# Kernel tuning notes

Hardware: AMD Instinct MI355X
Metric: run time of the kernel (lower is better)

Reference implementation:

```python
import jax, jax.numpy as jnp
import numpy as np

N = 2_000_000
VOXEL_SIZE = (0.1, 0.1, 0.1)
PC_RANGE = (-50.0, -50.0, -5.0, 50.0, 50.0, 3.0)
NUM_BATCHES = 4


def setup_inputs() -> dict:
    key = jax.random.key(0)
    k1, k2 = jax.random.split(key)
    pmin = jnp.array(PC_RANGE[:3], dtype=jnp.float32)
    pmax = jnp.array(PC_RANGE[3:], dtype=jnp.float32)
    # points uniformly distributed over the configured point-cloud range
    points = jax.random.uniform(k1, (N, 3), dtype=jnp.float32, minval=pmin, maxval=pmax)
    batch_indices = jnp.sort(jax.random.randint(k2, (N,), 0, NUM_BATCHES, dtype=jnp.int32))
    return {"points": points, "batch_indices": batch_indices}


def reference(points, batch_indices):
    """Vectorized equivalent of PointVoxelizer.forward.

    Returns fixed-shape (jit-friendly) analogues of the torch outputs:
      voxel_coords   [N, 4] int32  [batch, z, y, x], padded rows = -1
      voxel_features [N, 3] float32 voxel centers, padded rows = 0
      point_to_voxel_map [N] int32, -1 for invalid points
      n_voxels       scalar int32, number of real (non-padding) voxels
    The per-batch torch.unique + offset concatenation is reproduced exactly by
    a single sorted unique over the combined hash batch*GRID + cell_hash,
    since unique sorts and the hash is lexicographic in (batch, x, y, z).
    """
    dtype = points.dtype
    vsize = jnp.array(VOXEL_SIZE, dtype=dtype)
    pmin = jnp.array(PC_RANGE[:3], dtype=dtype)
    pmax = jnp.array(PC_RANGE[3:], dtype=dtype)

    vc = jnp.floor((points - pmin) / vsize).astype(jnp.int32)  # [N,3] (x,y,z)
    grid = jnp.ceil((pmax - pmin) / vsize).astype(jnp.int32)   # [3] = (1000,1000,80)
    valid = jnp.all(vc >= 0, axis=1) & jnp.all(vc < grid, axis=1)  # [N]

    YZ = grid[1] * grid[2]
    GXYZ = grid[0] * YZ  # cells per batch element (8e7 < 2^31/NUM_BATCHES)
    cell_hash = vc[:, 0] * YZ + vc[:, 1] * grid[2] + vc[:, 2]
    SENTINEL = jnp.iinfo(jnp.int32).max
    combined = jnp.where(valid, batch_indices.astype(jnp.int32) * GXYZ + cell_hash, SENTINEL)

    uniq, inv = jnp.unique(combined, return_inverse=True, size=N, fill_value=SENTINEL)
    is_real = uniq != SENTINEL  # padding (and any invalid-point bucket) masked out

    point_to_voxel_map = jnp.where(valid, inv.reshape(-1).astype(jnp.int32), -1)

    b = uniq // GXYZ
    rem = uniq % GXYZ
    x = rem // YZ
    y = (rem % YZ) // grid[2]
    z = rem % grid[2]

    coords_bzyx = jnp.stack([b, z, y, x], axis=1).astype(jnp.int32)  # [N,4]
    voxel_coords = jnp.where(is_real[:, None], coords_bzyx, -1)

    xyz = jnp.stack([x, y, z], axis=1).astype(dtype)
    centers = pmin + (xyz + 0.5) * vsize
    voxel_features = jnp.where(is_real[:, None], centers, jnp.zeros((), dtype))

    n_voxels = is_real.sum().astype(jnp.int32)
    return voxel_coords, voxel_features, point_to_voxel_map, n_voxels
```

## Files before the change

### kernel.cpp

```cpp
#include <hip/hip_runtime.h>


namespace {

constexpr int GX = 1000, GY = 1000, GZ = 80;
constexpr int YZ = GY * GZ;
constexpr int GXYZ = GX * YZ;
constexpr int TOTAL_CELLS = GXYZ * 4;
constexpr int BBITS = 18;
constexpr int BCELLS = 1 << BBITS;
constexpr int NB = (TOTAL_CELLS + BCELLS - 1) >> BBITS;
constexpr int BWORDS = BCELLS / 32;
constexpr int NCHUNK = 512;
static_assert(NCHUNK % 64 == 0, "k2a wave scan");
static_assert(NB <= 2048, "1-block scans assume <=2048 elements");

constexpr size_t OFF_PK    = 8000000;
constexpr size_t OFF_POS   = 16000000;
constexpr size_t OFF_MVAL  = 24000000;
constexpr size_t OFF_DK    = 32000000;
constexpr size_t OFF_HIST  = 40000000;
constexpr size_t OFF_TOT   = 43000000;
constexpr size_t OFF_BOFF  = 43100000;
constexpr size_t OFF_DCNT  = 43200000;
constexpr size_t OFF_DRANK = 43300000;

__device__ __forceinline__ int sw(int w) {
  return ((w & 7) << 10) | (w >> 3);
}

__global__ void k1_keys_hist(const float* __restrict__ pts, const int* __restrict__ bi,
                             unsigned* __restrict__ upt, unsigned* __restrict__ hist,
                             int n, int cpb) {
  __shared__ unsigned h[NB];
  const int c = blockIdx.x;
  for (int b = threadIdx.x; b < NB; b += blockDim.x) h[b] = 0;
  __syncthreads();
  const int lo = c * cpb, hi = min(n, lo + cpb);
  for (int i = lo + threadIdx.x; i < hi; i += blockDim.x) {
    float px = pts[3 * i + 0], py = pts[3 * i + 1], pz = pts[3 * i + 2];
    int vx = (int)floorf((px + 50.0f) / 0.1f);
    int vy = (int)floorf((py + 50.0f) / 0.1f);
    int vz = (int)floorf((pz + 5.0f) / 0.1f);
    bool valid = (vx >= 0) & (vy >= 0) & (vz >= 0) & (vx < GX) & (vy < GY) & (vz < GZ);
    unsigned u = 0xFFFFFFFFu;
    if (valid) {
      u = (unsigned)(bi[i] * GXYZ + vx * YZ + vy * GZ + vz);
      atomicAdd(&h[u >> BBITS], 1u);
    }
    upt[i] = u;
  }
  __syncthreads();
  for (int b = threadIdx.x; b < NB; b += blockDim.x)
    hist[(size_t)c * NB + b] = h[b];
}

__global__ void k2a_chunk_pre(unsigned* __restrict__ hist, unsigned* __restrict__ tot) {
  const int wid = (blockIdx.x * blockDim.x + threadIdx.x) >> 6;
  const int lane = threadIdx.x & 63;
  if (wid >= NB) return;
  unsigned run = 0;
  for (int c0 = 0; c0 < NCHUNK; c0 += 64) {
    const size_t idx = (size_t)(c0 + lane) * NB + wid;
    unsigned v = hist[idx];
    unsigned inc = v;
    for (int o = 1; o < 64; o <<= 1) {
      unsigned t = __shfl_up(inc, o);
      if (lane >= o) inc += t;
    }
    hist[idx] = run + inc - v;
    run += __shfl(inc, 63);
  }
  if (lane == 63) tot[wid] = run;
}

__device__ __forceinline__ void scan_block_2048(const unsigned* __restrict__ src,
                                                unsigned* __restrict__ dst, int nb,
                                                bool write_end, float* out_total) {
  __shared__ unsigned s16[16];
  const int tid = threadIdx.x;
  const int lane = tid & 63, wid = tid >> 6;
  unsigned v0 = (2 * tid     < nb) ? src[2 * tid]     : 0u;
  unsigned v1 = (2 * tid + 1 < nb) ? src[2 * tid + 1] : 0u;
  unsigned t = v0 + v1;
  unsigned incl = t;
  #pragma unroll
  for (int o = 1; o < 64; o <<= 1) {
    unsigned u = __shfl_up(incl, o);
    if (lane >= o) incl += u;
  }
  if (lane == 63) s16[wid] = incl;
  __syncthreads();
  unsigned woff = 0;
  for (int j = 0; j < wid; j++) woff += s16[j];
  unsigned excl = woff + incl - t;
  if (2 * tid     < nb) dst[2 * tid]     = excl;
  if (2 * tid + 1 < nb) dst[2 * tid + 1] = excl + v0;
  if (tid == 1023) {
    if (write_end) dst[nb] = excl + t;
    if (out_total) *out_total = (float)(excl + t);
  }
}

__global__ void __launch_bounds__(1024) k2b_scan_tot(const unsigned* __restrict__ tot,
                                                     unsigned* __restrict__ boff) {
  scan_block_2048(tot, boff, NB, true, nullptr);
}

__global__ void __launch_bounds__(1024) k5_scan_dcnt(const unsigned* __restrict__ dcnt,
                                                     unsigned* __restrict__ drank_tbl,
                                                     float* __restrict__ out_nvox) {
  scan_block_2048(dcnt, drank_tbl, NB, false, out_nvox);
}

__global__ void k3_scatter(const unsigned* __restrict__ upt, const unsigned* __restrict__ hist,
                           const unsigned* __restrict__ boff, unsigned* __restrict__ pk,
                           unsigned* __restrict__ pos, int n, int cpb) {
  __shared__ unsigned cur[NB];
  const int c = blockIdx.x;
  for (int b = threadIdx.x; b < NB; b += blockDim.x)
    cur[b] = boff[b] + hist[(size_t)c * NB + b];
  __syncthreads();
  const int lo = c * cpb, hi = min(n, lo + cpb);
  for (int i = lo + threadIdx.x; i < hi; i += blockDim.x) {
    unsigned u = upt[i];
    if (u == 0xFFFFFFFFu) continue;
    unsigned p = atomicAdd(&cur[u >> BBITS], 1u);
    pk[p] = u;
    pos[i] = p;
  }
}

__global__ void __launch_bounds__(1024) k4_rank(
    const unsigned* __restrict__ pk, const unsigned* __restrict__ boff,
    unsigned* __restrict__ dcnt, unsigned* __restrict__ dk,
    unsigned* __restrict__ mapval) {
  __shared__ unsigned bits[BWORDS];
  __shared__ unsigned wpre[BWORDS];
  __shared__ unsigned s16[16];
  const int tid = threadIdx.x;
  const int bid = blockIdx.x;
  const int lane = tid & 63, wid = tid >> 6;

  for (int w = tid; w < BWORDS; w += 1024) bits[w] = 0;
  __syncthreads();
  const unsigned lo = boff[bid], hi = boff[bid + 1];
  const unsigned base = (unsigned)bid << BBITS;
  for (unsigned p = lo + tid; p < hi; p += 1024) {
    unsigned local = pk[p] - base;
    atomicOr(&bits[sw(local >> 5)], 1u << (local & 31));
  }
  __syncthreads();

  unsigned c8[8];
  unsigned t = 0;
  #pragma unroll
  for (int j = 0; j < 8; j++) {
    unsigned p = __popc(bits[j * 1024 + tid]);
    c8[j] = t;
    t += p;
  }
  unsigned incl = t;
  #pragma unroll
  for (int o = 1; o < 64; o <<= 1) {
    unsigned u = __shfl_up(incl, o);
    if (lane >= o) incl += u;
  }
  if (lane == 63) s16[wid] = incl;
  __syncthreads();
  unsigned woff = 0;
  for (int j = 0; j < wid; j++) woff += s16[j];
  const unsigned excl = woff + incl - t;
  #pragma unroll
  for (int j = 0; j < 8; j++) wpre[j * 1024 + tid] = excl + c8[j];
  if (tid == 1023) dcnt[bid] = excl + t;

  const unsigned dkb = lo;
  #pragma unroll
  for (int j = 0; j < 8; j++) {
    unsigned m = bits[j * 1024 + tid];
    unsigned r = excl + c8[j];
    const unsigned lbase = (unsigned)(tid * 8 + j) << 5;
    while (m) {
      int bit = __ffs(m) - 1;
      m &= m - 1;
      dk[dkb + r] = base + lbase + (unsigned)bit;
      r++;
    }
  }
  __syncthreads();

  for (unsigned p = lo + tid; p < hi; p += 1024) {
    unsigned local = pk[p] - base;
    int slot = sw((int)(local >> 5));
    mapval[p] = wpre[slot] + (unsigned)__popc(bits[slot] & ((1u << (local & 31)) - 1u));
  }
}

__global__ void k6_emit(const unsigned* __restrict__ dk, const unsigned* __restrict__ boff,
                        const unsigned* __restrict__ dcnt, const unsigned* __restrict__ drank_tbl,
                        const float* __restrict__ nvox_f,
                        float* __restrict__ out_coords, float* __restrict__ out_feats, int n) {
  const int tid = threadIdx.x;
  const int bid = blockIdx.x;

  if (bid >= NB) {
    const unsigned nv = (unsigned)*nvox_f;
    const int row = (bid - NB) * 256 + tid;
    if (row < n && (unsigned)row >= nv) {
      float* c = out_coords + (size_t)row * 4;
      c[0] = -1.0f; c[1] = -1.0f; c[2] = -1.0f; c[3] = -1.0f;
      float* f = out_feats + (size_t)row * 3;
      f[0] = 0.0f; f[1] = 0.0f; f[2] = 0.0f;
    }
    return;
  }

  const unsigned drank = drank_tbl[bid];
  const unsigned dc = dcnt[bid];
  const unsigned dkb = boff[bid];
  for (unsigned j = tid; j < dc; j += 256) {
    unsigned u = dk[dkb + j];
    int bat = (int)(u / (unsigned)GXYZ);
    int rem = (int)(u % (unsigned)GXYZ);
    int x = rem / YZ, ry = rem % YZ;
    int y = ry / GZ, z = ry % GZ;
    const size_t r = drank + j;
    float* cc = out_coords + r * 4;
    cc[0] = (float)bat; cc[1] = (float)z; cc[2] = (float)y; cc[3] = (float)x;
    float* ff = out_feats + r * 3;
    ff[0] = -50.0f + ((float)x + 0.5f) * 0.1f;
    ff[1] = -50.0f + ((float)y + 0.5f) * 0.1f;
    ff[2] = -5.0f + ((float)z + 0.5f) * 0.1f;
  }
}

__global__ void k7_map(const unsigned* __restrict__ upt, const unsigned* __restrict__ pos,
                       const unsigned* __restrict__ mapval, const unsigned* __restrict__ drank_tbl,
                       float* __restrict__ out_map, int n) {
  int i = blockIdx.x * blockDim.x + threadIdx.x;
  if (i >= n) return;
  unsigned u = upt[i];
  if (u == 0xFFFFFFFFu) {
    out_map[i] = -1.0f;
    return;
  }
  out_map[i] = (float)(drank_tbl[u >> BBITS] + mapval[pos[i]]);
}

}

extern "C" void kernel_launch(void* const* d_in, const int* in_sizes, int n_in,
                              void* d_out, int out_size, void* d_ws, size_t ws_size,
                              hipStream_t stream) {
  const int N = in_sizes[0] / 3;
  const float* pts = (const float*)d_in[0];
  const int* bi = (const int*)d_in[1];
  float* out = (float*)d_out;

  unsigned* upt   = (unsigned*)d_ws;
  unsigned* pk    = (unsigned*)((char*)d_ws + OFF_PK);
  unsigned* pos   = (unsigned*)((char*)d_ws + OFF_POS);
  unsigned* mval  = (unsigned*)((char*)d_ws + OFF_MVAL);
  unsigned* dk    = (unsigned*)((char*)d_ws + OFF_DK);
  unsigned* hist  = (unsigned*)((char*)d_ws + OFF_HIST);
  unsigned* tot   = (unsigned*)((char*)d_ws + OFF_TOT);
  unsigned* boff  = (unsigned*)((char*)d_ws + OFF_BOFF);
  unsigned* dcnt  = (unsigned*)((char*)d_ws + OFF_DCNT);
  unsigned* drank = (unsigned*)((char*)d_ws + OFF_DRANK);

  float* out_coords = out;
  float* out_feats  = out + 4LL * N;
  float* out_map    = out + 7LL * N;
  float* out_nvox   = out + 8LL * N;

  const int cpb = (N + NCHUNK - 1) / NCHUNK;
  const int pad_blocks = (N + 255) / 256;

  k1_keys_hist<<<NCHUNK, 256, 0, stream>>>(pts, bi, upt, hist, N, cpb);
  k2a_chunk_pre<<<(NB * 64 + 255) / 256, 256, 0, stream>>>(hist, tot);
  k2b_scan_tot<<<1, 1024, 0, stream>>>(tot, boff);
  k3_scatter<<<NCHUNK, 256, 0, stream>>>(upt, hist, boff, pk, pos, N, cpb);
  k4_rank<<<NB, 1024, 0, stream>>>(pk, boff, dcnt, dk, mval);
  k5_scan_dcnt<<<1, 1024, 0, stream>>>(dcnt, drank, out_nvox);
  k6_emit<<<NB + pad_blocks, 256, 0, stream>>>(dk, boff, dcnt, drank, out_nvox,
                                               out_coords, out_feats, N);
  k7_map<<<(N + 255) / 256, 256, 0, stream>>>(upt, pos, mval, drank, out_map, N);
}
```

Measured before the change: 175.3 us.

## Fold scans into neighbor kernels and merge emit with map pass

```diff
diff --git a/kernel.cpp b/kernel.cpp
--- a/kernel.cpp
+++ b/kernel.cpp
@@ -13,7 +13,8 @@
 constexpr int BWORDS = BCELLS / 32;
 constexpr int NCHUNK = 512;
 static_assert(NCHUNK % 64 == 0, "k2a wave scan");
-static_assert(NB <= 2048, "1-block scans assume <=2048 elements");
+static_assert(NB <= 1280, "k3 LDS scan: 256 thr x 5");
+static_assert(NB <= 2048, "k4 tail scan: 1024 thr x 2");
 
 constexpr size_t OFF_PK    = 8000000;
 constexpr size_t OFF_POS   = 16000000;
@@ -24,6 +25,7 @@
 constexpr size_t OFF_BOFF  = 43100000;
 constexpr size_t OFF_DCNT  = 43200000;
 constexpr size_t OFF_DRANK = 43300000;
+constexpr size_t OFF_CTR   = 43400000;
 
 __device__ __forceinline__ int sw(int w) {
   return ((w & 7) << 10) | (w >> 3);
@@ -31,9 +33,10 @@
 
 __global__ void k1_keys_hist(const float* __restrict__ pts, const int* __restrict__ bi,
                              unsigned* __restrict__ upt, unsigned* __restrict__ hist,
-                             int n, int cpb) {
+                             unsigned* __restrict__ ctr, int n, int cpb) {
   __shared__ unsigned h[NB];
   const int c = blockIdx.x;
+  if (c == 0 && threadIdx.x == 0) *ctr = 0;
   for (int b = threadIdx.x; b < NB; b += blockDim.x) h[b] = 0;
   __syncthreads();
   const int lo = c * cpb, hi = min(n, lo + cpb);
@@ -74,58 +77,55 @@
   if (lane == 63) tot[wid] = run;
 }
 
-__device__ __forceinline__ void scan_block_2048(const unsigned* __restrict__ src,
-                                                unsigned* __restrict__ dst, int nb,
-                                                bool write_end, float* out_total) {
-  __shared__ unsigned s16[16];
+__global__ void k3_scatter(const unsigned* __restrict__ upt, const unsigned* __restrict__ hist,
+                           const unsigned* __restrict__ tot, unsigned* __restrict__ boff,
+                           unsigned* __restrict__ pk, unsigned* __restrict__ pos,
+                           int n, int cpb) {
+  __shared__ unsigned arr[NB];
+  __shared__ unsigned s4w[4];
   const int tid = threadIdx.x;
-  const int lane = tid & 63, wid = tid >> 6;
-  unsigned v0 = (2 * tid     < nb) ? src[2 * tid]     : 0u;
-  unsigned v1 = (2 * tid + 1 < nb) ? src[2 * tid + 1] : 0u;
-  unsigned t = v0 + v1;
+  const int lane = tid & 63, wv = tid >> 6;
+  const int c = blockIdx.x;
+
+  unsigned lv[5];
+  unsigned t = 0;
+  #pragma unroll
+  for (int j = 0; j < 5; j++) {
+    int k = tid * 5 + j;
+    unsigned v = (k < NB) ? tot[k] : 0u;
+    lv[j] = t;
+    t += v;
+  }
   unsigned incl = t;
   #pragma unroll
   for (int o = 1; o < 64; o <<= 1) {
     unsigned u = __shfl_up(incl, o);
     if (lane >= o) incl += u;
   }
-  if (lane == 63) s16[wid] = incl;
+  if (lane == 63) s4w[wv] = incl;
   __syncthreads();
   unsigned woff = 0;
-  for (int j = 0; j < wid; j++) woff += s16[j];
+  for (int j = 0; j < wv; j++) woff += s4w[j];
   unsigned excl = woff + incl - t;
-  if (2 * tid     < nb) dst[2 * tid]     = excl;
-  if (2 * tid + 1 < nb) dst[2 * tid + 1] = excl + v0;
-  if (tid == 1023) {
-    if (write_end) dst[nb] = excl + t;
-    if (out_total) *out_total = (float)(excl + t);
-  }
-}
-
-__global__ void __launch_bounds__(1024) k2b_scan_tot(const unsigned* __restrict__ tot,
-                                                     unsigned* __restrict__ boff) {
-  scan_block_2048(tot, boff, NB, true, nullptr);
-}
-
-__global__ void __launch_bounds__(1024) k5_scan_dcnt(const unsigned* __restrict__ dcnt,
-                                                     unsigned* __restrict__ drank_tbl,
-                                                     float* __restrict__ out_nvox) {
-  scan_block_2048(dcnt, drank_tbl, NB, false, out_nvox);
-}
-
-__global__ void k3_scatter(const unsigned* __restrict__ upt, const unsigned* __restrict__ hist,
-                           const unsigned* __restrict__ boff, unsigned* __restrict__ pk,
-                           unsigned* __restrict__ pos, int n, int cpb) {
-  __shared__ unsigned cur[NB];
-  const int c = blockIdx.x;
-  for (int b = threadIdx.x; b < NB; b += blockDim.x)
-    cur[b] = boff[b] + hist[(size_t)c * NB + b];
-  __syncthreads();
+  #pragma unroll
+  for (int j = 0; j < 5; j++) {
+    int k = tid * 5 + j;
+    if (k < NB) arr[k] = excl + lv[j];
+  }
+  __syncthreads();
+  if (c == 0) {
+    for (int k = tid; k < NB; k += 256) boff[k] = arr[k];
+    if (tid == 0) boff[NB] = s4w[0] + s4w[1] + s4w[2] + s4w[3];
+  }
+  __syncthreads();
+  for (int b = tid; b < NB; b += 256) arr[b] += hist[(size_t)c * NB + b];
+  __syncthreads();
+
   const int lo = c * cpb, hi = min(n, lo + cpb);
-  for (int i = lo + threadIdx.x; i < hi; i += blockDim.x) {
+  for (int i = lo + tid; i < hi; i += 256) {
     unsigned u = upt[i];
     if (u == 0xFFFFFFFFu) continue;
-    unsigned p = atomicAdd(&cur[u >> BBITS], 1u);
+    unsigned p = atomicAdd(&arr[u >> BBITS], 1u);
     pk[p] = u;
     pos[i] = p;
   }
@@ -134,10 +134,12 @@
 __global__ void __launch_bounds__(1024) k4_rank(
     const unsigned* __restrict__ pk, const unsigned* __restrict__ boff,
     unsigned* __restrict__ dcnt, unsigned* __restrict__ dk,
-    unsigned* __restrict__ mapval) {
+    unsigned* __restrict__ mapval, unsigned* __restrict__ ctr,
+    unsigned* __restrict__ drank_tbl, float* __restrict__ out_nvox) {
   __shared__ unsigned bits[BWORDS];
   __shared__ unsigned wpre[BWORDS];
   __shared__ unsigned s16[16];
+  __shared__ unsigned lastF;
   const int tid = threadIdx.x;
   const int bid = blockIdx.x;
   const int lane = tid & 63, wid = tid >> 6;
@@ -195,57 +197,83 @@
     int slot = sw((int)(local >> 5));
     mapval[p] = wpre[slot] + (unsigned)__popc(bits[slot] & ((1u << (local & 31)) - 1u));
   }
-}
-
-__global__ void k6_emit(const unsigned* __restrict__ dk, const unsigned* __restrict__ boff,
-                        const unsigned* __restrict__ dcnt, const unsigned* __restrict__ drank_tbl,
-                        const float* __restrict__ nvox_f,
-                        float* __restrict__ out_coords, float* __restrict__ out_feats, int n) {
+
+  __syncthreads();
+  if (tid == 0) {
+    __threadfence();
+    lastF = (atomicAdd(ctr, 1u) == (unsigned)(NB - 1)) ? 1u : 0u;
+  }
+  __syncthreads();
+  if (lastF) {
+    unsigned v0 = (2 * tid < NB)
+        ? __hip_atomic_load(&dcnt[2 * tid], __ATOMIC_RELAXED, __HIP_MEMORY_SCOPE_AGENT) : 0u;
+    unsigned v1 = (2 * tid + 1 < NB)
+        ? __hip_atomic_load(&dcnt[2 * tid + 1], __ATOMIC_RELAXED, __HIP_MEMORY_SCOPE_AGENT) : 0u;
+    unsigned t2 = v0 + v1;
+    unsigned inc2 = t2;
+    #pragma unroll
+    for (int o = 1; o < 64; o <<= 1) {
+      unsigned u = __shfl_up(inc2, o);
+      if (lane >= o) inc2 += u;
+    }
+    if (lane == 63) s16[wid] = inc2;
+    __syncthreads();
+    unsigned w2 = 0;
+    for (int j = 0; j < wid; j++) w2 += s16[j];
+    unsigned e2 = w2 + inc2 - t2;
+    if (2 * tid < NB) drank_tbl[2 * tid] = e2;
+    if (2 * tid + 1 < NB) drank_tbl[2 * tid + 1] = e2 + v0;
+    if (tid == 1023) *out_nvox = (float)(e2 + t2);
+  }
+}
+
+__global__ void k6_emit_map(const unsigned* __restrict__ dk, const unsigned* __restrict__ boff,
+                            const unsigned* __restrict__ dcnt,
+                            const unsigned* __restrict__ drank_tbl,
+                            const unsigned* __restrict__ upt, const unsigned* __restrict__ pos,
+                            const unsigned* __restrict__ mapval,
+                            const float* __restrict__ nvox_f,
+                            float* __restrict__ out_coords, float* __restrict__ out_feats,
+                            float* __restrict__ out_map, int n) {
   const int tid = threadIdx.x;
   const int bid = blockIdx.x;
 
-  if (bid >= NB) {
-    const unsigned nv = (unsigned)*nvox_f;
-    const int row = (bid - NB) * 256 + tid;
-    if (row < n && (unsigned)row >= nv) {
-      float* c = out_coords + (size_t)row * 4;
-      c[0] = -1.0f; c[1] = -1.0f; c[2] = -1.0f; c[3] = -1.0f;
-      float* f = out_feats + (size_t)row * 3;
-      f[0] = 0.0f; f[1] = 0.0f; f[2] = 0.0f;
+  if (bid < NB) {
+    const unsigned drank = drank_tbl[bid];
+    const unsigned dc = dcnt[bid];
+    const unsigned dkb = boff[bid];
+    for (unsigned j = tid; j < dc; j += 256) {
+      unsigned u = dk[dkb + j];
+      int bat = (int)(u / (unsigned)GXYZ);
+      int rem = (int)(u % (unsigned)GXYZ);
+      int x = rem / YZ, ry = rem % YZ;
+      int y = ry / GZ, z = ry % GZ;
+      const size_t r = drank + j;
+      float* cc = out_coords + r * 4;
+      cc[0] = (float)bat; cc[1] = (float)z; cc[2] = (float)y; cc[3] = (float)x;
+      float* ff = out_feats + r * 3;
+      ff[0] = -50.0f + ((float)x + 0.5f) * 0.1f;
+      ff[1] = -50.0f + ((float)y + 0.5f) * 0.1f;
+      ff[2] = -5.0f + ((float)z + 0.5f) * 0.1f;
     }
     return;
   }
 
-  const unsigned drank = drank_tbl[bid];
-  const unsigned dc = dcnt[bid];
-  const unsigned dkb = boff[bid];
-  for (unsigned j = tid; j < dc; j += 256) {
-    unsigned u = dk[dkb + j];
-    int bat = (int)(u / (unsigned)GXYZ);
-    int rem = (int)(u % (unsigned)GXYZ);
-    int x = rem / YZ, ry = rem % YZ;
-    int y = ry / GZ, z = ry % GZ;
-    const size_t r = drank + j;
-    float* cc = out_coords + r * 4;
-    cc[0] = (float)bat; cc[1] = (float)z; cc[2] = (float)y; cc[3] = (float)x;
-    float* ff = out_feats + r * 3;
-    ff[0] = -50.0f + ((float)x + 0.5f) * 0.1f;
-    ff[1] = -50.0f + ((float)y + 0.5f) * 0.1f;
-    ff[2] = -5.0f + ((float)z + 0.5f) * 0.1f;
-  }
-}
-
-__global__ void k7_map(const unsigned* __restrict__ upt, const unsigned* __restrict__ pos,
-                       const unsigned* __restrict__ mapval, const unsigned* __restrict__ drank_tbl,
-                       float* __restrict__ out_map, int n) {
-  int i = blockIdx.x * blockDim.x + threadIdx.x;
+  const int i = (bid - NB) * 256 + tid;
   if (i >= n) return;
   unsigned u = upt[i];
   if (u == 0xFFFFFFFFu) {
     out_map[i] = -1.0f;
-    return;
-  }
-  out_map[i] = (float)(drank_tbl[u >> BBITS] + mapval[pos[i]]);
+  } else {
+    out_map[i] = (float)(drank_tbl[u >> BBITS] + mapval[pos[i]]);
+  }
+  const unsigned nv = (unsigned)*nvox_f;
+  if ((unsigned)i >= nv) {
+    float* c = out_coords + (size_t)i * 4;
+    c[0] = -1.0f; c[1] = -1.0f; c[2] = -1.0f; c[3] = -1.0f;
+    float* f = out_feats + (size_t)i * 3;
+    f[0] = 0.0f; f[1] = 0.0f; f[2] = 0.0f;
+  }
 }
 
 }
@@ -268,6 +296,7 @@
   unsigned* boff  = (unsigned*)((char*)d_ws + OFF_BOFF);
   unsigned* dcnt  = (unsigned*)((char*)d_ws + OFF_DCNT);
   unsigned* drank = (unsigned*)((char*)d_ws + OFF_DRANK);
+  unsigned* ctr   = (unsigned*)((char*)d_ws + OFF_CTR);
 
   float* out_coords = out;
   float* out_feats  = out + 4LL * N;
@@ -275,15 +304,13 @@
   float* out_nvox   = out + 8LL * N;
 
   const int cpb = (N + NCHUNK - 1) / NCHUNK;
-  const int pad_blocks = (N + 255) / 256;
-
-  k1_keys_hist<<<NCHUNK, 256, 0, stream>>>(pts, bi, upt, hist, N, cpb);
+  const int row_blocks = (N + 255) / 256;
+
+  k1_keys_hist<<<NCHUNK, 256, 0, stream>>>(pts, bi, upt, hist, ctr, N, cpb);
   k2a_chunk_pre<<<(NB * 64 + 255) / 256, 256, 0, stream>>>(hist, tot);
-  k2b_scan_tot<<<1, 1024, 0, stream>>>(tot, boff);
-  k3_scatter<<<NCHUNK, 256, 0, stream>>>(upt, hist, boff, pk, pos, N, cpb);
-  k4_rank<<<NB, 1024, 0, stream>>>(pk, boff, dcnt, dk, mval);
-  k5_scan_dcnt<<<1, 1024, 0, stream>>>(dcnt, drank, out_nvox);
-  k6_emit<<<NB + pad_blocks, 256, 0, stream>>>(dk, boff, dcnt, drank, out_nvox,
-                                               out_coords, out_feats, N);
-  k7_map<<<(N + 255) / 256, 256, 0, stream>>>(upt, pos, mval, drank, out_map, N);
-}
+  k3_scatter<<<NCHUNK, 256, 0, stream>>>(upt, hist, tot, boff, pk, pos, N, cpb);
+  k4_rank<<<NB, 1024, 0, stream>>>(pk, boff, dcnt, dk, mval, ctr, drank, out_nvox);
+  k6_emit_map<<<NB + row_blocks, 256, 0, stream>>>(dk, boff, dcnt, drank, upt, pos,
+                                                   mval, out_nvox, out_coords,
+                                                   out_feats, out_map, N);
+}
```

Measured after the change: 214.9 us. 22.6% more time.
